# Kernel optimization log

Hardware: AMD Instinct MI355X
Metric: run time of the kernel (lower is better)

## Reference

```python
import jax, jax.numpy as jnp
import numpy as np

B, S, D, OUT = 32, 2048, 1024, 4096
EPS = 1e-6


def setup_inputs() -> dict:
    key = jax.random.key(0)
    ks = jax.random.split(key, 6)
    x = jax.random.normal(ks[0], (B, S, D), dtype=jnp.float32)
    ln_w = jnp.ones((D,), dtype=jnp.float32)
    att_w = jax.random.normal(ks[1], (D, 1), dtype=jnp.float32) * (1.0 / np.sqrt(D))
    att_b = jnp.zeros((1,), dtype=jnp.float32)
    geglu_w = jax.random.normal(ks[2], (D, 2 * OUT), dtype=jnp.float32) * (1.0 / np.sqrt(D))
    geglu_b = jnp.zeros((2 * OUT,), dtype=jnp.float32)
    return {"x": x, "ln_w": ln_w, "att_w": att_w, "att_b": att_b,
            "geglu_w": geglu_w, "geglu_b": geglu_b}


def reference(x, ln_w, att_w, att_b, geglu_w, geglu_b):
    # T5LayerNorm: RMS norm, no mean subtraction
    var = jnp.mean(jnp.square(x), axis=-1, keepdims=True)  # [B,S,1]
    xn = x * jax.lax.rsqrt(var + EPS) * ln_w               # [B,S,D]
    # Attention pooling with learned scoring vector
    scores = jnp.einsum('bsd,dk->bsk', xn, att_w) + att_b   # [B,S,1]
    w = jax.nn.softmax(scores, axis=1)                      # softmax over seq
    pooled = jnp.einsum('bsk,bsd->bd', w, xn)               # [B,D]
    # GeGLU readout: value * gelu(gate)
    h = pooled @ geglu_w + geglu_b                          # [B,2*OUT]
    val, gate = jnp.split(h, 2, axis=-1)
    return val * jax.nn.gelu(gate, approximate=False)       # [B,OUT]
```

## Files before the change

### kernel.cpp

```cpp
#include <hip/hip_runtime.h>
#include <math.h>

#define B_    32
#define S_    2048
#define D_    1024
#define OUT_  4096
#define PB_   32
#define SLOT_ 1032
#define DSP_  8
#define CBL_  64

typedef float f32x4 __attribute__((ext_vector_type(4)));

template <int CTRL>
__device__ __forceinline__ float dpp_add(float s) {
    int t = __builtin_amdgcn_update_dpp(0, __builtin_bit_cast(int, s),
                                        CTRL, 0xF, 0xF, true);
    return s + __builtin_bit_cast(float, t);
}
__device__ __forceinline__ float rowred16(float s) {
    s = dpp_add<0x128>(s);
    s = dpp_add<0x124>(s);
    s = dpp_add<0x122>(s);
    s = dpp_add<0x121>(s);
    return s;
}
__device__ __forceinline__ float xgroup4(float s) {
    float a = __builtin_bit_cast(float, __builtin_amdgcn_readlane(__builtin_bit_cast(int, s),  0));
    float b = __builtin_bit_cast(float, __builtin_amdgcn_readlane(__builtin_bit_cast(int, s), 16));
    float c = __builtin_bit_cast(float, __builtin_amdgcn_readlane(__builtin_bit_cast(int, s), 32));
    float d = __builtin_bit_cast(float, __builtin_amdgcn_readlane(__builtin_bit_cast(int, s), 48));
    return (a + b) + (c + d);
}

__global__ __launch_bounds__(256, 4) void k_pass1(
    const float* __restrict__ x, const float* __restrict__ ln_w,
    const float* __restrict__ att_w, const float* __restrict__ att_b,
    float* __restrict__ partA)
{
    const int b    = blockIdx.x / PB_;
    const int p    = blockIdx.x % PB_;
    const int tid  = threadIdx.x;
    const int lane = tid & 63;
    const int wv   = tid >> 6;

    float4 av[4];
#pragma unroll
    for (int jj = 0; jj < 4; ++jj) {
        const int d4 = (jj * 64 + lane) * 4;
        float4 lw = *(const float4*)(ln_w + d4);
        float4 aw = *(const float4*)(att_w + d4);
        av[jj] = make_float4(lw.x * aw.x, lw.y * aw.y, lw.z * aw.z, lw.w * aw.w);
    }
    const float ab = att_b[0];

    float  m = -INFINITY, l = 0.f;
    float4 pacc[4];
#pragma unroll
    for (int jj = 0; jj < 4; ++jj) pacc[jj] = make_float4(0.f, 0.f, 0.f, 0.f);

    const int s0 = p * 64 + wv * 16;
    const float* xb = x + ((size_t)b * S_ + s0) * D_;

    for (int pr = 0; pr < 4; ++pr) {
        const float* xr = xb + (size_t)(pr * 4) * D_;
        float4 x0[4], x1[4], x2[4], x3[4];
        float ss0 = 0.f, ss1 = 0.f, ss2 = 0.f, ss3 = 0.f;
        float dt0 = 0.f, dt1 = 0.f, dt2 = 0.f, dt3 = 0.f;
#pragma unroll
        for (int jj = 0; jj < 4; ++jj) {
            const int off = (jj * 64 + lane) * 4;
            x0[jj] = *(const float4*)(xr + off);
            x1[jj] = *(const float4*)(xr + D_ + off);
            x2[jj] = *(const float4*)(xr + 2 * D_ + off);
            x3[jj] = *(const float4*)(xr + 3 * D_ + off);
        }
#pragma unroll
        for (int jj = 0; jj < 4; ++jj) {
            ss0 += x0[jj].x*x0[jj].x + x0[jj].y*x0[jj].y + x0[jj].z*x0[jj].z + x0[jj].w*x0[jj].w;
            dt0 += x0[jj].x*av[jj].x + x0[jj].y*av[jj].y + x0[jj].z*av[jj].z + x0[jj].w*av[jj].w;
            ss1 += x1[jj].x*x1[jj].x + x1[jj].y*x1[jj].y + x1[jj].z*x1[jj].z + x1[jj].w*x1[jj].w;
            dt1 += x1[jj].x*av[jj].x + x1[jj].y*av[jj].y + x1[jj].z*av[jj].z + x1[jj].w*av[jj].w;
            ss2 += x2[jj].x*x2[jj].x + x2[jj].y*x2[jj].y + x2[jj].z*x2[jj].z + x2[jj].w*x2[jj].w;
            dt2 += x2[jj].x*av[jj].x + x2[jj].y*av[jj].y + x2[jj].z*av[jj].z + x2[jj].w*av[jj].w;
            ss3 += x3[jj].x*x3[jj].x + x3[jj].y*x3[jj].y + x3[jj].z*x3[jj].z + x3[jj].w*x3[jj].w;
            dt3 += x3[jj].x*av[jj].x + x3[jj].y*av[jj].y + x3[jj].z*av[jj].z + x3[jj].w*av[jj].w;
        }
        ss0 = xgroup4(rowred16(ss0)); dt0 = xgroup4(rowred16(dt0));
        ss1 = xgroup4(rowred16(ss1)); dt1 = xgroup4(rowred16(dt1));
        ss2 = xgroup4(rowred16(ss2)); dt2 = xgroup4(rowred16(dt2));
        ss3 = xgroup4(rowred16(ss3)); dt3 = xgroup4(rowred16(dt3));

        const float rr0 = rsqrtf(ss0 * (1.f / (float)D_) + 1e-6f);
        const float rr1 = rsqrtf(ss1 * (1.f / (float)D_) + 1e-6f);
        const float rr2 = rsqrtf(ss2 * (1.f / (float)D_) + 1e-6f);
        const float rr3 = rsqrtf(ss3 * (1.f / (float)D_) + 1e-6f);
        const float sc0 = dt0 * rr0 + ab;
        const float sc1 = dt1 * rr1 + ab;
        const float sc2 = dt2 * rr2 + ab;
        const float sc3 = dt3 * rr3 + ab;
        const float nm  = fmaxf(fmaxf(m, fmaxf(sc0, sc1)), fmaxf(sc2, sc3));
        const float c   = expf(m - nm);
        const float w0  = expf(sc0 - nm);
        const float w1  = expf(sc1 - nm);
        const float w2  = expf(sc2 - nm);
        const float w3  = expf(sc3 - nm);
        l = l * c + ((w0 + w1) + (w2 + w3));
        const float a0 = w0 * rr0, a1 = w1 * rr1, a2 = w2 * rr2, a3 = w3 * rr3;
#pragma unroll
        for (int jj = 0; jj < 4; ++jj) {
            float tx = fmaf(x0[jj].x, a0, fmaf(x1[jj].x, a1, fmaf(x2[jj].x, a2, x3[jj].x * a3)));
            float ty = fmaf(x0[jj].y, a0, fmaf(x1[jj].y, a1, fmaf(x2[jj].y, a2, x3[jj].y * a3)));
            float tz = fmaf(x0[jj].z, a0, fmaf(x1[jj].z, a1, fmaf(x2[jj].z, a2, x3[jj].z * a3)));
            float tw = fmaf(x0[jj].w, a0, fmaf(x1[jj].w, a1, fmaf(x2[jj].w, a2, x3[jj].w * a3)));
            pacc[jj].x = fmaf(pacc[jj].x, c, tx);
            pacc[jj].y = fmaf(pacc[jj].y, c, ty);
            pacc[jj].z = fmaf(pacc[jj].z, c, tz);
            pacc[jj].w = fmaf(pacc[jj].w, c, tw);
        }
        m = nm;
    }

    __shared__ float s_m[4];
    __shared__ float s_l[4];
    __shared__ float s_pacc[4][D_];
    if (lane == 0) { s_m[wv] = m; s_l[wv] = l; }
#pragma unroll
    for (int jj = 0; jj < 4; ++jj)
        *(float4*)&s_pacc[wv][(jj * 64 + lane) * 4] = pacc[jj];
    __syncthreads();

    const float M = fmaxf(fmaxf(s_m[0], s_m[1]), fmaxf(s_m[2], s_m[3]));
    float  Lg = 0.f;
    float4 acc = make_float4(0.f, 0.f, 0.f, 0.f);
#pragma unroll
    for (int w = 0; w < 4; ++w) {
        const float cc = expf(s_m[w] - M);
        Lg += cc * s_l[w];
        const float4 v = *(const float4*)&s_pacc[w][tid * 4];
        acc.x += cc * v.x; acc.y += cc * v.y; acc.z += cc * v.z; acc.w += cc * v.w;
    }
    float* slot = partA + (size_t)blockIdx.x * SLOT_;
    if (tid == 0) { slot[0] = M; slot[1] = Lg; }
    *(float4*)(slot + 8 + tid * 4) = acc;
}

__global__ __launch_bounds__(256) void k_combine(
    const float* __restrict__ partA, const float* __restrict__ ln_w,
    float* __restrict__ pooled)
{
    const int b   = blockIdx.x >> 2;
    const int dq  = blockIdx.x & 3;
    const int tid = threadIdx.x;
    const int d   = dq * 256 + tid;
    const float* base = partA + (size_t)b * PB_ * SLOT_;

    float M = -INFINITY;
#pragma unroll 8
    for (int p = 0; p < PB_; ++p) M = fmaxf(M, base[(size_t)p * SLOT_]);

    float Lg = 0.f, acc = 0.f;
    for (int p = 0; p < PB_; ++p) {
        const float* sl = base + (size_t)p * SLOT_;
        const float c = expf(sl[0] - M);
        Lg  += c * sl[1];
        acc += c * sl[8 + d];
    }
    pooled[(size_t)b * D_ + d] = acc / Lg * ln_w[d];
}

#define LOADW(WV, WG, dq_) do {                                               \
    _Pragma("unroll") for (int i = 0; i < 4; ++i) {                           \
        WV[i] = Wb[(size_t)((dq_) * 4 + i) * (2 * OUT_) + j];                 \
        WG[i] = Wb[(size_t)((dq_) * 4 + i) * (2 * OUT_) + OUT_ + j];          \
    } } while (0)

#define GFMA(WV, WG, dq_) do {                                                \
    _Pragma("unroll") for (int k = 0; k < 8; ++k) {                           \
        const f32x4 p4 = *(const f32x4*)&sp[g * 8 + k][(dq_) * 4];            \
        accv[k] += p4.x*WV[0] + p4.y*WV[1] + p4.z*WV[2] + p4.w*WV[3];         \
        accg[k] += p4.x*WG[0] + p4.y*WG[1] + p4.z*WG[2] + p4.w*WG[3];         \
    } } while (0)

__global__ __launch_bounds__(256) void k_gemm(
    const float* __restrict__ pooled, const float* __restrict__ W,
    float* __restrict__ partC)
{
    const int cb  = blockIdx.x % CBL_;
    const int ds  = blockIdx.x / CBL_;
    const int tid = threadIdx.x;
    const int j   = tid & 63;
    const int g   = tid >> 6;

    __shared__ float sp[B_][132];
    for (int i = tid; i < B_ * 128; i += 256) {
        const int bb = i >> 7, dd = i & 127;
        sp[bb][dd] = pooled[(size_t)bb * D_ + ds * 128 + dd];
    }
    __syncthreads();

    float accv[8], accg[8];
#pragma unroll
    for (int k = 0; k < 8; ++k) { accv[k] = 0.f; accg[k] = 0.f; }

    const float* Wb = W + (size_t)(ds * 128) * (2 * OUT_) + cb * 64;
    float wva[4], wga[4], wvb[4], wgb[4];
    LOADW(wva, wga, 0);
    for (int h = 0; h < 16; ++h) {
        LOADW(wvb, wgb, 2 * h + 1);
        GFMA(wva, wga, 2 * h);
        if (h < 15) LOADW(wva, wga, 2 * h + 2);
        GFMA(wvb, wgb, 2 * h + 1);
    }

#pragma unroll
    for (int k = 0; k < 8; ++k) {
        const int bb = g * 8 + k;
        float* outp = partC + ((size_t)ds * B_ + bb) * (2 * OUT_) + cb * 64;
        outp[j]        = accv[k];
        outp[OUT_ + j] = accg[k];
    }
}

__global__ __launch_bounds__(256) void k_finish(
    const float* __restrict__ partC, const float* __restrict__ gb,
    float* __restrict__ out)
{
    const int idx = blockIdx.x * 256 + threadIdx.x;
    const int b = idx >> 12;
    const int o = idx & (OUT_ - 1);
    float v = gb[o];
    float g = gb[OUT_ + o];
#pragma unroll
    for (int ds = 0; ds < DSP_; ++ds) {
        const float* pc = partC + ((size_t)ds * B_ + b) * (2 * OUT_);
        v += pc[o];
        g += pc[OUT_ + o];
    }
    const float gelu = 0.5f * g * (1.f + erff(g * 0.70710678118654752f));
    out[idx] = v * gelu;
}

extern "C" void kernel_launch(void* const* d_in, const int* in_sizes, int n_in,
                              void* d_out, int out_size, void* d_ws, size_t ws_size,
                              hipStream_t stream) {
    const float* x     = (const float*)d_in[0];
    const float* ln_w  = (const float*)d_in[1];
    const float* att_w = (const float*)d_in[2];
    const float* att_b = (const float*)d_in[3];
    const float* gw    = (const float*)d_in[4];
    const float* gb    = (const float*)d_in[5];
    float* out = (float*)d_out;

    float* ws     = (float*)d_ws;
    float* partA  = ws;
    float* pooled = partA + (size_t)B_ * PB_ * SLOT_;
    float* partC  = pooled + (size_t)B_ * D_;

    hipLaunchKernelGGL(k_pass1,   dim3(B_ * PB_),          dim3(256), 0, stream,
                       x, ln_w, att_w, att_b, partA);
    hipLaunchKernelGGL(k_combine, dim3(B_ * 4),            dim3(256), 0, stream,
                       partA, ln_w, pooled);
    hipLaunchKernelGGL(k_gemm,    dim3(CBL_ * DSP_),       dim3(256), 0, stream,
                       pooled, gw, partC);
    hipLaunchKernelGGL(k_finish,  dim3((B_ * OUT_) / 256), dim3(256), 0, stream,
                       partC, gb, out);
}
```

Measured before the change: 94.92 us.

## Split pass1 into more blocks with single-shot rows per wave

Pass1 now launches 64 blocks per batch with 512 threads, and each wave handles only 4 rows, loaded once up front instead of looping over 16 rows with an online softmax. This raises memory-level parallelism and removes the serial dependent loop, so more x loads are in flight across the GPU. In exchange, the partial buffer doubles, and the combine kernel must reduce 64 partials per batch instead of 32.

```diff
diff --git a/kernel.cpp b/kernel.cpp
--- a/kernel.cpp
+++ b/kernel.cpp
@@ -5,12 +5,13 @@
 #define S_    2048
 #define D_    1024
 #define OUT_  4096
-#define PB_   32
+#define PB2_  64
 #define SLOT_ 1032
 #define DSP_  8
 #define CBL_  64
 
 typedef float f32x4 __attribute__((ext_vector_type(4)));
+typedef float f32x2 __attribute__((ext_vector_type(2)));
 
 template <int CTRL>
 __device__ __forceinline__ float dpp_add(float s) {
@@ -33,116 +34,106 @@
     return (a + b) + (c + d);
 }
 
-__global__ __launch_bounds__(256, 4) void k_pass1(
+__global__ __launch_bounds__(512, 4) void k_pass1(
     const float* __restrict__ x, const float* __restrict__ ln_w,
     const float* __restrict__ att_w, const float* __restrict__ att_b,
     float* __restrict__ partA)
 {
-    const int b    = blockIdx.x / PB_;
-    const int p    = blockIdx.x % PB_;
+    const int b    = blockIdx.x >> 6;
+    const int p    = blockIdx.x & 63;
     const int tid  = threadIdx.x;
     const int lane = tid & 63;
     const int wv   = tid >> 6;
 
-    float4 av[4];
-#pragma unroll
-    for (int jj = 0; jj < 4; ++jj) {
-        const int d4 = (jj * 64 + lane) * 4;
-        float4 lw = *(const float4*)(ln_w + d4);
-        float4 aw = *(const float4*)(att_w + d4);
-        av[jj] = make_float4(lw.x * aw.x, lw.y * aw.y, lw.z * aw.z, lw.w * aw.w);
+    const int s0 = p * 32 + wv * 4;
+    const float* xr = x + ((size_t)b * S_ + s0) * D_;
+
+    f32x4 x0[4], x1[4], x2[4], x3[4];
+#pragma unroll
+    for (int c = 0; c < 4; ++c) {
+        const int off = (c * 64 + lane) * 4;
+        x0[c] = *(const f32x4*)(xr + off);
+        x1[c] = *(const f32x4*)(xr + D_ + off);
+        x2[c] = *(const f32x4*)(xr + 2 * D_ + off);
+        x3[c] = *(const f32x4*)(xr + 3 * D_ + off);
+    }
+
+    f32x4 av[4];
+#pragma unroll
+    for (int c = 0; c < 4; ++c) {
+        const int d4 = (c * 64 + lane) * 4;
+        f32x4 lw = *(const f32x4*)(ln_w + d4);
+        f32x4 aw = *(const f32x4*)(att_w + d4);
+        av[c] = lw * aw;
     }
     const float ab = att_b[0];
 
-    float  m = -INFINITY, l = 0.f;
-    float4 pacc[4];
-#pragma unroll
-    for (int jj = 0; jj < 4; ++jj) pacc[jj] = make_float4(0.f, 0.f, 0.f, 0.f);
-
-    const int s0 = p * 64 + wv * 16;
-    const float* xb = x + ((size_t)b * S_ + s0) * D_;
-
-    for (int pr = 0; pr < 4; ++pr) {
-        const float* xr = xb + (size_t)(pr * 4) * D_;
-        float4 x0[4], x1[4], x2[4], x3[4];
-        float ss0 = 0.f, ss1 = 0.f, ss2 = 0.f, ss3 = 0.f;
-        float dt0 = 0.f, dt1 = 0.f, dt2 = 0.f, dt3 = 0.f;
-#pragma unroll
-        for (int jj = 0; jj < 4; ++jj) {
-            const int off = (jj * 64 + lane) * 4;
-            x0[jj] = *(const float4*)(xr + off);
-            x1[jj] = *(const float4*)(xr + D_ + off);
-            x2[jj] = *(const float4*)(xr + 2 * D_ + off);
-            x3[jj] = *(const float4*)(xr + 3 * D_ + off);
-        }
-#pragma unroll
-        for (int jj = 0; jj < 4; ++jj) {
-            ss0 += x0[jj].x*x0[jj].x + x0[jj].y*x0[jj].y + x0[jj].z*x0[jj].z + x0[jj].w*x0[jj].w;
-            dt0 += x0[jj].x*av[jj].x + x0[jj].y*av[jj].y + x0[jj].z*av[jj].z + x0[jj].w*av[jj].w;
-            ss1 += x1[jj].x*x1[jj].x + x1[jj].y*x1[jj].y + x1[jj].z*x1[jj].z + x1[jj].w*x1[jj].w;
-            dt1 += x1[jj].x*av[jj].x + x1[jj].y*av[jj].y + x1[jj].z*av[jj].z + x1[jj].w*av[jj].w;
-            ss2 += x2[jj].x*x2[jj].x + x2[jj].y*x2[jj].y + x2[jj].z*x2[jj].z + x2[jj].w*x2[jj].w;
-            dt2 += x2[jj].x*av[jj].x + x2[jj].y*av[jj].y + x2[jj].z*av[jj].z + x2[jj].w*av[jj].w;
-            ss3 += x3[jj].x*x3[jj].x + x3[jj].y*x3[jj].y + x3[jj].z*x3[jj].z + x3[jj].w*x3[jj].w;
-            dt3 += x3[jj].x*av[jj].x + x3[jj].y*av[jj].y + x3[jj].z*av[jj].z + x3[jj].w*av[jj].w;
-        }
-        ss0 = xgroup4(rowred16(ss0)); dt0 = xgroup4(rowred16(dt0));
-        ss1 = xgroup4(rowred16(ss1)); dt1 = xgroup4(rowred16(dt1));
-        ss2 = xgroup4(rowred16(ss2)); dt2 = xgroup4(rowred16(dt2));
-        ss3 = xgroup4(rowred16(ss3)); dt3 = xgroup4(rowred16(dt3));
-
-        const float rr0 = rsqrtf(ss0 * (1.f / (float)D_) + 1e-6f);
-        const float rr1 = rsqrtf(ss1 * (1.f / (float)D_) + 1e-6f);
-        const float rr2 = rsqrtf(ss2 * (1.f / (float)D_) + 1e-6f);
-        const float rr3 = rsqrtf(ss3 * (1.f / (float)D_) + 1e-6f);
-        const float sc0 = dt0 * rr0 + ab;
-        const float sc1 = dt1 * rr1 + ab;
-        const float sc2 = dt2 * rr2 + ab;
-        const float sc3 = dt3 * rr3 + ab;
-        const float nm  = fmaxf(fmaxf(m, fmaxf(sc0, sc1)), fmaxf(sc2, sc3));
-        const float c   = expf(m - nm);
-        const float w0  = expf(sc0 - nm);
-        const float w1  = expf(sc1 - nm);
-        const float w2  = expf(sc2 - nm);
-        const float w3  = expf(sc3 - nm);
-        l = l * c + ((w0 + w1) + (w2 + w3));
-        const float a0 = w0 * rr0, a1 = w1 * rr1, a2 = w2 * rr2, a3 = w3 * rr3;
-#pragma unroll
-        for (int jj = 0; jj < 4; ++jj) {
-            float tx = fmaf(x0[jj].x, a0, fmaf(x1[jj].x, a1, fmaf(x2[jj].x, a2, x3[jj].x * a3)));
-            float ty = fmaf(x0[jj].y, a0, fmaf(x1[jj].y, a1, fmaf(x2[jj].y, a2, x3[jj].y * a3)));
-            float tz = fmaf(x0[jj].z, a0, fmaf(x1[jj].z, a1, fmaf(x2[jj].z, a2, x3[jj].z * a3)));
-            float tw = fmaf(x0[jj].w, a0, fmaf(x1[jj].w, a1, fmaf(x2[jj].w, a2, x3[jj].w * a3)));
-            pacc[jj].x = fmaf(pacc[jj].x, c, tx);
-            pacc[jj].y = fmaf(pacc[jj].y, c, ty);
-            pacc[jj].z = fmaf(pacc[jj].z, c, tz);
-            pacc[jj].w = fmaf(pacc[jj].w, c, tw);
-        }
-        m = nm;
-    }
-
-    __shared__ float s_m[4];
-    __shared__ float s_l[4];
-    __shared__ float s_pacc[4][D_];
-    if (lane == 0) { s_m[wv] = m; s_l[wv] = l; }
-#pragma unroll
-    for (int jj = 0; jj < 4; ++jj)
-        *(float4*)&s_pacc[wv][(jj * 64 + lane) * 4] = pacc[jj];
+    float ss0 = 0.f, ss1 = 0.f, ss2 = 0.f, ss3 = 0.f;
+    float dt0 = 0.f, dt1 = 0.f, dt2 = 0.f, dt3 = 0.f;
+#pragma unroll
+    for (int c = 0; c < 4; ++c) {
+        ss0 += x0[c].x*x0[c].x + x0[c].y*x0[c].y + x0[c].z*x0[c].z + x0[c].w*x0[c].w;
+        dt0 += x0[c].x*av[c].x + x0[c].y*av[c].y + x0[c].z*av[c].z + x0[c].w*av[c].w;
+        ss1 += x1[c].x*x1[c].x + x1[c].y*x1[c].y + x1[c].z*x1[c].z + x1[c].w*x1[c].w;
+        dt1 += x1[c].x*av[c].x + x1[c].y*av[c].y + x1[c].z*av[c].z + x1[c].w*av[c].w;
+        ss2 += x2[c].x*x2[c].x + x2[c].y*x2[c].y + x2[c].z*x2[c].z + x2[c].w*x2[c].w;
+        dt2 += x2[c].x*av[c].x + x2[c].y*av[c].y + x2[c].z*av[c].z + x2[c].w*av[c].w;
+        ss3 += x3[c].x*x3[c].x + x3[c].y*x3[c].y + x3[c].z*x3[c].z + x3[c].w*x3[c].w;
+        dt3 += x3[c].x*av[c].x + x3[c].y*av[c].y + x3[c].z*av[c].z + x3[c].w*av[c].w;
+    }
+    ss0 = xgroup4(rowred16(ss0)); dt0 = xgroup4(rowred16(dt0));
+    ss1 = xgroup4(rowred16(ss1)); dt1 = xgroup4(rowred16(dt1));
+    ss2 = xgroup4(rowred16(ss2)); dt2 = xgroup4(rowred16(dt2));
+    ss3 = xgroup4(rowred16(ss3)); dt3 = xgroup4(rowred16(dt3));
+
+    const float rr0 = rsqrtf(ss0 * (1.f / (float)D_) + 1e-6f);
+    const float rr1 = rsqrtf(ss1 * (1.f / (float)D_) + 1e-6f);
+    const float rr2 = rsqrtf(ss2 * (1.f / (float)D_) + 1e-6f);
+    const float rr3 = rsqrtf(ss3 * (1.f / (float)D_) + 1e-6f);
+    const float sc0 = dt0 * rr0 + ab;
+    const float sc1 = dt1 * rr1 + ab;
+    const float sc2 = dt2 * rr2 + ab;
+    const float sc3 = dt3 * rr3 + ab;
+    const float nm  = fmaxf(fmaxf(sc0, sc1), fmaxf(sc2, sc3));
+    const float w0  = expf(sc0 - nm);
+    const float w1  = expf(sc1 - nm);
+    const float w2  = expf(sc2 - nm);
+    const float w3  = expf(sc3 - nm);
+    const float l   = (w0 + w1) + (w2 + w3);
+    const float a0 = w0 * rr0, a1 = w1 * rr1, a2 = w2 * rr2, a3 = w3 * rr3;
+
+    f32x4 pacc[4];
+#pragma unroll
+    for (int c = 0; c < 4; ++c) {
+        pacc[c].x = fmaf(x0[c].x, a0, fmaf(x1[c].x, a1, fmaf(x2[c].x, a2, x3[c].x * a3)));
+        pacc[c].y = fmaf(x0[c].y, a0, fmaf(x1[c].y, a1, fmaf(x2[c].y, a2, x3[c].y * a3)));
+        pacc[c].z = fmaf(x0[c].z, a0, fmaf(x1[c].z, a1, fmaf(x2[c].z, a2, x3[c].z * a3)));
+        pacc[c].w = fmaf(x0[c].w, a0, fmaf(x1[c].w, a1, fmaf(x2[c].w, a2, x3[c].w * a3)));
+    }
+
+    __shared__ float s_m[8];
+    __shared__ float s_l[8];
+    __shared__ float s_pacc[8][D_];
+    if (lane == 0) { s_m[wv] = nm; s_l[wv] = l; }
+#pragma unroll
+    for (int c = 0; c < 4; ++c)
+        *(f32x4*)&s_pacc[wv][(c * 64 + lane) * 4] = pacc[c];
     __syncthreads();
 
-    const float M = fmaxf(fmaxf(s_m[0], s_m[1]), fmaxf(s_m[2], s_m[3]));
-    float  Lg = 0.f;
-    float4 acc = make_float4(0.f, 0.f, 0.f, 0.f);
-#pragma unroll
-    for (int w = 0; w < 4; ++w) {
+    const float M = fmaxf(fmaxf(fmaxf(s_m[0], s_m[1]), fmaxf(s_m[2], s_m[3])),
+                          fmaxf(fmaxf(s_m[4], s_m[5]), fmaxf(s_m[6], s_m[7])));
+    float Lg = 0.f;
+    f32x2 acc = (f32x2){0.f, 0.f};
+#pragma unroll
+    for (int w = 0; w < 8; ++w) {
         const float cc = expf(s_m[w] - M);
         Lg += cc * s_l[w];
-        const float4 v = *(const float4*)&s_pacc[w][tid * 4];
-        acc.x += cc * v.x; acc.y += cc * v.y; acc.z += cc * v.z; acc.w += cc * v.w;
+        const f32x2 v = *(const f32x2*)&s_pacc[w][tid * 2];
+        acc.x += cc * v.x; acc.y += cc * v.y;
     }
     float* slot = partA + (size_t)blockIdx.x * SLOT_;
     if (tid == 0) { slot[0] = M; slot[1] = Lg; }
-    *(float4*)(slot + 8 + tid * 4) = acc;
+    *(f32x2*)(slot + 8 + tid * 2) = acc;
 }
 
 __global__ __launch_bounds__(256) void k_combine(
@@ -153,14 +144,14 @@
     const int dq  = blockIdx.x & 3;
     const int tid = threadIdx.x;
     const int d   = dq * 256 + tid;
-    const float* base = partA + (size_t)b * PB_ * SLOT_;
+    const float* base = partA + (size_t)b * PB2_ * SLOT_;
 
     float M = -INFINITY;
 #pragma unroll 8
-    for (int p = 0; p < PB_; ++p) M = fmaxf(M, base[(size_t)p * SLOT_]);
+    for (int p = 0; p < PB2_; ++p) M = fmaxf(M, base[(size_t)p * SLOT_]);
 
     float Lg = 0.f, acc = 0.f;
-    for (int p = 0; p < PB_; ++p) {
+    for (int p = 0; p < PB2_; ++p) {
         const float* sl = base + (size_t)p * SLOT_;
         const float c = expf(sl[0] - M);
         Lg  += c * sl[1];
@@ -254,10 +245,10 @@
 
     float* ws     = (float*)d_ws;
     float* partA  = ws;
-    float* pooled = partA + (size_t)B_ * PB_ * SLOT_;
+    float* pooled = partA + (size_t)B_ * PB2_ * SLOT_;
     float* partC  = pooled + (size_t)B_ * D_;
 
-    hipLaunchKernelGGL(k_pass1,   dim3(B_ * PB_),          dim3(256), 0, stream,
+    hipLaunchKernelGGL(k_pass1,   dim3(B_ * PB2_),         dim3(512), 0, stream,
                        x, ln_w, att_w, att_b, partA);
     hipLaunchKernelGGL(k_combine, dim3(B_ * 4),            dim3(256), 0, stream,
                        partA, ln_w, pooled);
```

New measurement: 103.9 us. +9.5%, slower.
